# Kernel tuning notes

Hardware: AMD Instinct MI355X
Metric: run time of the kernel (lower is better)

The kernel has to match this reference:

```python
import jax, jax.numpy as jnp
import numpy as np

OUT = 2048        # weight_size[0]
IN_BASE = 2048    # original input features
N_EMBED = 64      # replacements per iteration
IN_TOT = IN_BASE + 2 * N_EMBED  # 2176, weight_size[1]
NNZ_W = 400000
NNZ_B = 1024
BATCH = 8192


def setup_inputs() -> dict:
    key = jax.random.key(0)
    ks = jax.random.split(key, 10)
    return {
        "x": jax.random.normal(ks[0], (BATCH, IN_BASE), dtype=jnp.float32),
        "weight_vals": jax.random.normal(ks[1], (NNZ_W,), dtype=jnp.float32),
        "weight_rows": jax.random.randint(ks[2], (NNZ_W,), 0, OUT, dtype=jnp.int32),
        "weight_cols": jax.random.randint(ks[3], (NNZ_W,), 0, IN_TOT, dtype=jnp.int32),
        "bias_vals": jax.random.normal(ks[4], (NNZ_B,), dtype=jnp.float32),
        "bias_idx": jax.random.randint(ks[5], (NNZ_B,), 0, OUT, dtype=jnp.int32),
        "embed0_vals": jax.random.uniform(ks[6], (N_EMBED,), dtype=jnp.float32),
        "embed0_parents": jax.random.randint(ks[7], (N_EMBED,), 0, IN_BASE, dtype=jnp.int32),
        "embed1_vals": jax.random.uniform(ks[8], (N_EMBED,), dtype=jnp.float32),
        "embed1_parents": jax.random.randint(ks[9], (N_EMBED,), 0, IN_BASE + N_EMBED, dtype=jnp.int32),
    }


def reference(x, weight_vals, weight_rows, weight_cols, bias_vals, bias_idx,
              embed0_vals, embed0_parents, embed1_vals, embed1_parents):
    # EmbedLinear layers: each appends one new feature per stored row,
    # new_feat[:, c] = value[c] * x[:, parent[c]]  (single nnz per sparse row)
    x = jnp.concatenate([x, x[:, embed0_parents] * embed0_vals[None, :]], axis=1)  # [B, 2112]
    x = jnp.concatenate([x, x[:, embed1_parents] * embed1_vals[None, :]], axis=1)  # [B, 2176]
    # sparse weight -> dense via scatter-add (coalesce semantics sum duplicates)
    W = jnp.zeros((OUT, IN_TOT), dtype=weight_vals.dtype).at[weight_rows, weight_cols].add(weight_vals)
    b = jnp.zeros((OUT,), dtype=bias_vals.dtype).at[bias_idx].add(bias_vals)
    # (W @ x^T)^T + b  ==  x @ W^T + b
    return x @ W.T + b[None, :]
```

## Files before the change

kernel.cpp:

```cpp
#include <hip/hip_runtime.h>
#include <stdint.h>

#define OUT_F   2048
#define IN_BASE 2048
#define N_EMB   64
#define IN_TOT  2176
#define NNZ_W   400000
#define NNZ_B   1024
#define BATCH   8192

typedef __bf16 bf16x8 __attribute__((ext_vector_type(8)));
typedef __bf16 bf16x4 __attribute__((ext_vector_type(4)));
typedef float  floatx16 __attribute__((ext_vector_type(16)));

__global__ void __launch_bounds__(256) build_x_kernel(
    const float* __restrict__ x,
    const float* __restrict__ e0v, const int* __restrict__ e0p,
    const float* __restrict__ e1v, const int* __restrict__ e1p,
    __bf16* __restrict__ xb)
{
    const int GROUPS = IN_TOT / 4;
    int gid = blockIdx.x * 256 + threadIdx.x;
    int b = gid / GROUPS;
    int g = gid - b * GROUPS;
    const float* xr = x + (size_t)b * IN_BASE;

    float v[4];
    if (g < IN_BASE / 4) {
        const float4 t = *(const float4*)(xr + g * 4);
        v[0] = t.x; v[1] = t.y; v[2] = t.z; v[3] = t.w;
    } else if (g < (IN_BASE + N_EMB) / 4) {
        int j = (g - IN_BASE / 4) * 4;
#pragma unroll
        for (int t = 0; t < 4; t++) v[t] = e0v[j + t] * xr[e0p[j + t]];
    } else {
        int j = (g - (IN_BASE + N_EMB) / 4) * 4;
#pragma unroll
        for (int t = 0; t < 4; t++) {
            int p = e1p[j + t];
            float base = (p < IN_BASE) ? xr[p]
                                       : e0v[p - IN_BASE] * xr[e0p[p - IN_BASE]];
            v[t] = e1v[j + t] * base;
        }
    }
    bf16x4 o;
    o[0] = (__bf16)v[0]; o[1] = (__bf16)v[1]; o[2] = (__bf16)v[2]; o[3] = (__bf16)v[3];
    *(bf16x4*)(xb + (size_t)b * IN_TOT + g * 4) = o;
}

__global__ void __launch_bounds__(256) scatter_kernel(
    const float* __restrict__ wv, const int* __restrict__ wr,
    const int* __restrict__ wc,
    const float* __restrict__ bv, const int* __restrict__ bi,
    float* __restrict__ Wf, float* __restrict__ bf)
{
    int i = blockIdx.x * 256 + threadIdx.x;
    if (i < NNZ_W) {
        atomicAdd(Wf + (size_t)wr[i] * IN_TOT + wc[i], wv[i]);
    } else if (i < NNZ_W + NNZ_B) {
        int j = i - NNZ_W;
        atomicAdd(bf + bi[j], bv[j]);
    }
}

__global__ void __launch_bounds__(256) w_to_bf16_kernel(
    const float* __restrict__ Wf, __bf16* __restrict__ Wb)
{
    int e = (blockIdx.x * 256 + threadIdx.x) * 4;
    const float4 t = *(const float4*)(Wf + e);
    bf16x4 o;
    o[0] = (__bf16)t.x; o[1] = (__bf16)t.y; o[2] = (__bf16)t.z; o[3] = (__bf16)t.w;
    *(bf16x4*)(Wb + e) = o;
}

#define BM 128
#define BN 128
#define BK 64

__global__ void __launch_bounds__(256) gemm_kernel(
    const __bf16* __restrict__ A,
    const __bf16* __restrict__ W,
    const float*  __restrict__ bias,
    float* __restrict__ C)
{
    __shared__ __bf16 sA[BM * BK];
    __shared__ __bf16 sB[BN * BK];

    const int tid   = threadIdx.x;
    const int bm    = blockIdx.x;
    const int bn    = blockIdx.y;
    const int wave  = tid >> 6;
    const int lane  = tid & 63;
    const int wm    = (wave >> 1) * 64;
    const int wn    = (wave & 1) * 64;
    const int l32   = lane & 31;
    const int khalf = lane >> 5;

    floatx16 acc[2][2] = {};

    const int srow   = tid >> 3;
    const int kchunk = ((tid & 7) ^ ((tid >> 3) & 7)) * 8;
    const __bf16* Ag = A + (size_t)(bm * BM + srow) * IN_TOT + kchunk;
    const __bf16* Wg = W + (size_t)(bn * BN + srow) * IN_TOT + kchunk;
    char* sAb = (char*)sA;
    char* sBb = (char*)sB;

    for (int k0 = 0; k0 < IN_TOT; k0 += BK) {
#pragma unroll
        for (int i = 0; i < 4; i++) {
            __builtin_amdgcn_global_load_lds(
                (__attribute__((address_space(1))) void*)(uintptr_t)(Ag + (size_t)i * 32 * IN_TOT + k0),
                (__attribute__((address_space(3))) void*)(sAb + i * 4096 + tid * 16),
                16, 0, 0);
            __builtin_amdgcn_global_load_lds(
                (__attribute__((address_space(1))) void*)(uintptr_t)(Wg + (size_t)i * 32 * IN_TOT + k0),
                (__attribute__((address_space(3))) void*)(sBb + i * 4096 + tid * 16),
                16, 0, 0);
        }
        __syncthreads();

#pragma unroll
        for (int ks = 0; ks < 4; ks++) {
            const int sl = ((ks * 2 + khalf) ^ (l32 & 7)) * 8;
            bf16x8 af[2], bfr[2];
#pragma unroll
            for (int mi = 0; mi < 2; mi++)
                af[mi] = *(const bf16x8*)(sA + (wm + mi * 32 + l32) * BK + sl);
#pragma unroll
            for (int ni = 0; ni < 2; ni++)
                bfr[ni] = *(const bf16x8*)(sB + (wn + ni * 32 + l32) * BK + sl);
#pragma unroll
            for (int mi = 0; mi < 2; mi++)
#pragma unroll
                for (int ni = 0; ni < 2; ni++)
                    acc[mi][ni] = __builtin_amdgcn_mfma_f32_32x32x16_bf16(
                        af[mi], bfr[ni], acc[mi][ni], 0, 0, 0);
        }
        __syncthreads();
    }

#pragma unroll
    for (int mi = 0; mi < 2; mi++) {
#pragma unroll
        for (int ni = 0; ni < 2; ni++) {
            const int colg = bn * BN + wn + ni * 32 + l32;
            const float bv = bias[colg];
            const int rowb = bm * BM + wm + mi * 32 + 4 * khalf;
#pragma unroll
            for (int reg = 0; reg < 16; reg++) {
                const int rowg = rowb + (reg & 3) + 8 * (reg >> 2);
                C[(size_t)rowg * OUT_F + colg] = acc[mi][ni][reg] + bv;
            }
        }
    }
}

extern "C" void kernel_launch(void* const* d_in, const int* in_sizes, int n_in,
                              void* d_out, int out_size, void* d_ws, size_t ws_size,
                              hipStream_t stream) {
    const float* x      = (const float*)d_in[0];
    const float* w_vals = (const float*)d_in[1];
    const int*   w_rows = (const int*)  d_in[2];
    const int*   w_cols = (const int*)  d_in[3];
    const float* b_vals = (const float*)d_in[4];
    const int*   b_idx  = (const int*)  d_in[5];
    const float* e0v    = (const float*)d_in[6];
    const int*   e0p    = (const int*)  d_in[7];
    const float* e1v    = (const float*)d_in[8];
    const int*   e1p    = (const int*)  d_in[9];
    float* out = (float*)d_out;

    char* ws = (char*)d_ws;
    const size_t W_F32_BYTES  = (size_t)OUT_F * IN_TOT * 4;
    const size_t B_F32_BYTES  = (size_t)OUT_F * 4;
    const size_t W_BF16_BYTES = (size_t)OUT_F * IN_TOT * 2;
    float*  Wf = (float*)ws;
    float*  bf = (float*)(ws + W_F32_BYTES);
    __bf16* Wb = (__bf16*)(ws + W_F32_BYTES + B_F32_BYTES);
    __bf16* xb = (__bf16*)(ws + W_F32_BYTES + B_F32_BYTES + W_BF16_BYTES);

    hipMemsetAsync(Wf, 0, W_F32_BYTES + B_F32_BYTES, stream);

    build_x_kernel<<<(BATCH * (IN_TOT / 4)) / 256, 256, 0, stream>>>(
        x, e0v, e0p, e1v, e1p, xb);

    scatter_kernel<<<(NNZ_W + NNZ_B + 255) / 256, 256, 0, stream>>>(
        w_vals, w_rows, w_cols, b_vals, b_idx, Wf, bf);

    w_to_bf16_kernel<<<((size_t)OUT_F * IN_TOT / 4) / 256, 256, 0, stream>>>(Wf, Wb);

    dim3 grid(BATCH / BM, OUT_F / BN);
    gemm_kernel<<<grid, 256, 0, stream>>>(xb, Wb, bf, out);
}
```

Before: 249.3 us.

## Fuse prep kernels and rebuild GEMM as 256x256 double-buffered 8-wave pipeline

Merges the x-build and scatter kernels into one launch and switches the atomics to unsafeAtomicAdd, which allows hardware float atomics. Rewrites the GEMM with 256x256 tiles, 512 threads and two LDS buffers. Global-to-LDS loads for upcoming K-tiles are interleaved with MFMA phases under fine-grained barriers and s_setprio, to hide load latency and raise arithmetic intensity. The larger tiles use 128KB of LDS per block and give only 256 blocks, so occupancy is low and tail balance gets worse.

Measured after the change: 260.7 us. 4.6% more time.

```diff
diff --git a/kernel.cpp b/kernel.cpp
--- a/kernel.cpp
+++ b/kernel.cpp
@@ -13,53 +13,58 @@
 typedef __bf16 bf16x4 __attribute__((ext_vector_type(4)));
 typedef float  floatx16 __attribute__((ext_vector_type(16)));
 
-__global__ void __launch_bounds__(256) build_x_kernel(
+#define AS1 __attribute__((address_space(1)))
+#define AS3 __attribute__((address_space(3)))
+
+#define NB_BUILD (BATCH * (IN_TOT / 4) / 256)
+#define NB_SCAT  ((NNZ_W + NNZ_B + 255) / 256)
+
+__global__ void __launch_bounds__(256) prep_kernel(
     const float* __restrict__ x,
     const float* __restrict__ e0v, const int* __restrict__ e0p,
     const float* __restrict__ e1v, const int* __restrict__ e1p,
-    __bf16* __restrict__ xb)
-{
-    const int GROUPS = IN_TOT / 4;
-    int gid = blockIdx.x * 256 + threadIdx.x;
-    int b = gid / GROUPS;
-    int g = gid - b * GROUPS;
-    const float* xr = x + (size_t)b * IN_BASE;
-
-    float v[4];
-    if (g < IN_BASE / 4) {
-        const float4 t = *(const float4*)(xr + g * 4);
-        v[0] = t.x; v[1] = t.y; v[2] = t.z; v[3] = t.w;
-    } else if (g < (IN_BASE + N_EMB) / 4) {
-        int j = (g - IN_BASE / 4) * 4;
-#pragma unroll
-        for (int t = 0; t < 4; t++) v[t] = e0v[j + t] * xr[e0p[j + t]];
-    } else {
-        int j = (g - (IN_BASE + N_EMB) / 4) * 4;
-#pragma unroll
-        for (int t = 0; t < 4; t++) {
-            int p = e1p[j + t];
-            float base = (p < IN_BASE) ? xr[p]
-                                       : e0v[p - IN_BASE] * xr[e0p[p - IN_BASE]];
-            v[t] = e1v[j + t] * base;
-        }
-    }
-    bf16x4 o;
-    o[0] = (__bf16)v[0]; o[1] = (__bf16)v[1]; o[2] = (__bf16)v[2]; o[3] = (__bf16)v[3];
-    *(bf16x4*)(xb + (size_t)b * IN_TOT + g * 4) = o;
-}
-
-__global__ void __launch_bounds__(256) scatter_kernel(
+    __bf16* __restrict__ xb,
     const float* __restrict__ wv, const int* __restrict__ wr,
     const int* __restrict__ wc,
     const float* __restrict__ bv, const int* __restrict__ bi,
-    float* __restrict__ Wf, float* __restrict__ bf)
+    float* __restrict__ Wf, float* __restrict__ bfp)
 {
-    int i = blockIdx.x * 256 + threadIdx.x;
-    if (i < NNZ_W) {
-        atomicAdd(Wf + (size_t)wr[i] * IN_TOT + wc[i], wv[i]);
-    } else if (i < NNZ_W + NNZ_B) {
-        int j = i - NNZ_W;
-        atomicAdd(bf + bi[j], bv[j]);
+    if (blockIdx.x < NB_BUILD) {
+        const int GROUPS = IN_TOT / 4;
+        int gid = blockIdx.x * 256 + threadIdx.x;
+        int b = gid / GROUPS;
+        int g = gid - b * GROUPS;
+        const float* xr = x + (size_t)b * IN_BASE;
+
+        float v[4];
+        if (g < IN_BASE / 4) {
+            const float4 t = *(const float4*)(xr + g * 4);
+            v[0] = t.x; v[1] = t.y; v[2] = t.z; v[3] = t.w;
+        } else if (g < (IN_BASE + N_EMB) / 4) {
+            int j = (g - IN_BASE / 4) * 4;
+#pragma unroll
+            for (int t = 0; t < 4; t++) v[t] = e0v[j + t] * xr[e0p[j + t]];
+        } else {
+            int j = (g - (IN_BASE + N_EMB) / 4) * 4;
+#pragma unroll
+            for (int t = 0; t < 4; t++) {
+                int p = e1p[j + t];
+                float base = (p < IN_BASE) ? xr[p]
+                                           : e0v[p - IN_BASE] * xr[e0p[p - IN_BASE]];
+                v[t] = e1v[j + t] * base;
+            }
+        }
+        bf16x4 o;
+        o[0] = (__bf16)v[0]; o[1] = (__bf16)v[1]; o[2] = (__bf16)v[2]; o[3] = (__bf16)v[3];
+        *(bf16x4*)(xb + (size_t)b * IN_TOT + g * 4) = o;
+    } else {
+        int i = (blockIdx.x - NB_BUILD) * 256 + threadIdx.x;
+        if (i < NNZ_W) {
+            unsafeAtomicAdd(Wf + (size_t)wr[i] * IN_TOT + wc[i], wv[i]);
+        } else if (i < NNZ_W + NNZ_B) {
+            int j = i - NNZ_W;
+            unsafeAtomicAdd(bfp + bi[j], bv[j]);
+        }
     }
 }
 
@@ -73,84 +78,122 @@
     *(bf16x4*)(Wb + e) = o;
 }
 
-#define BM 128
-#define BN 128
+#define BM 256
+#define BN 256
 #define BK 64
-
-__global__ void __launch_bounds__(256) gemm_kernel(
+#define NKT (IN_TOT / BK)
+static_assert(NKT % 2 == 0, "pipeline consumes K-tiles in pairs");
+
+#define CFENCE asm volatile("" ::: "memory")
+#define BAR do { CFENCE; __builtin_amdgcn_s_barrier(); CFENCE; } while (0)
+#define VMW(n) asm volatile("s_waitcnt vmcnt(" #n ")" ::: "memory")
+#define NOPS do {} while (0)
+
+#define STAGE(G, SBC, buf, tile, half) do {                                     \
+    const __bf16* _s = (G) + (size_t)((half) * 128) * IN_TOT + (tile) * 64;     \
+    char* _d = (SBC) + (buf) * 32768 + (half) * 16384 + tid * 16;               \
+    __builtin_amdgcn_global_load_lds((AS1 void*)(uintptr_t)_s,                  \
+                                     (AS3 void*)_d, 16, 0, 0);                  \
+    __builtin_amdgcn_global_load_lds((AS1 void*)(uintptr_t)(_s + (size_t)64 * IN_TOT), \
+                                     (AS3 void*)(_d + 8192), 16, 0, 0);         \
+} while (0)
+
+#define PHASE(buf, m, n, STG, WT) do {                                          \
+    const __bf16* _pA = sA + (buf) * 16384;                                     \
+    const __bf16* _pB = sB + (buf) * 16384;                                     \
+    bf16x8 _af[2][4], _bv[4];                                                   \
+    _Pragma("unroll") for (int ks = 0; ks < 4; ks++) {                          \
+        const int kc = ks * 2 + khalf;                                          \
+        _Pragma("unroll") for (int mi = 0; mi < 2; mi++) {                      \
+            const int r = (m) * 128 + wm * 64 + mi * 32 + l32;                  \
+            _af[mi][ks] = *(const bf16x8*)(_pA + r * 64 + ((kc ^ (r & 7)) * 8));\
+        }                                                                       \
+        const int rb = (n) * 128 + wn * 32 + l32;                               \
+        _bv[ks] = *(const bf16x8*)(_pB + rb * 64 + ((kc ^ (rb & 7)) * 8));      \
+    }                                                                           \
+    STG;                                                                        \
+    WT;                                                                         \
+    BAR;                                                                        \
+    __builtin_amdgcn_s_setprio(1);                                              \
+    _Pragma("unroll") for (int mi = 0; mi < 2; mi++)                            \
+        _Pragma("unroll") for (int ks = 0; ks < 4; ks++)                        \
+            acc[m][mi][n] = __builtin_amdgcn_mfma_f32_32x32x16_bf16(            \
+                _af[mi][ks], _bv[ks], acc[m][mi][n], 0, 0, 0);                  \
+    __builtin_amdgcn_s_setprio(0);                                              \
+    BAR;                                                                        \
+} while (0)
+
+__global__ void __launch_bounds__(512, 2) gemm_kernel(
     const __bf16* __restrict__ A,
     const __bf16* __restrict__ W,
     const float*  __restrict__ bias,
     float* __restrict__ C)
 {
-    __shared__ __bf16 sA[BM * BK];
-    __shared__ __bf16 sB[BN * BK];
+    __shared__ __align__(16) __bf16 sA[2 * 256 * 64];
+    __shared__ __align__(16) __bf16 sB[2 * 256 * 64];
 
     const int tid   = threadIdx.x;
     const int bm    = blockIdx.x;
     const int bn    = blockIdx.y;
     const int wave  = tid >> 6;
     const int lane  = tid & 63;
-    const int wm    = (wave >> 1) * 64;
-    const int wn    = (wave & 1) * 64;
+    const int wm    = wave >> 2;
+    const int wn    = wave & 3;
     const int l32   = lane & 31;
     const int khalf = lane >> 5;
 
-    floatx16 acc[2][2] = {};
+    floatx16 acc[2][2][2] = {};
 
     const int srow   = tid >> 3;
     const int kchunk = ((tid & 7) ^ ((tid >> 3) & 7)) * 8;
     const __bf16* Ag = A + (size_t)(bm * BM + srow) * IN_TOT + kchunk;
     const __bf16* Wg = W + (size_t)(bn * BN + srow) * IN_TOT + kchunk;
-    char* sAb = (char*)sA;
-    char* sBb = (char*)sB;
-
-    for (int k0 = 0; k0 < IN_TOT; k0 += BK) {
-#pragma unroll
-        for (int i = 0; i < 4; i++) {
-            __builtin_amdgcn_global_load_lds(
-                (__attribute__((address_space(1))) void*)(uintptr_t)(Ag + (size_t)i * 32 * IN_TOT + k0),
-                (__attribute__((address_space(3))) void*)(sAb + i * 4096 + tid * 16),
-                16, 0, 0);
-            __builtin_amdgcn_global_load_lds(
-                (__attribute__((address_space(1))) void*)(uintptr_t)(Wg + (size_t)i * 32 * IN_TOT + k0),
-                (__attribute__((address_space(3))) void*)(sBb + i * 4096 + tid * 16),
-                16, 0, 0);
-        }
-        __syncthreads();
-
-#pragma unroll
-        for (int ks = 0; ks < 4; ks++) {
-            const int sl = ((ks * 2 + khalf) ^ (l32 & 7)) * 8;
-            bf16x8 af[2], bfr[2];
-#pragma unroll
-            for (int mi = 0; mi < 2; mi++)
-                af[mi] = *(const bf16x8*)(sA + (wm + mi * 32 + l32) * BK + sl);
-#pragma unroll
-            for (int ni = 0; ni < 2; ni++)
-                bfr[ni] = *(const bf16x8*)(sB + (wn + ni * 32 + l32) * BK + sl);
-#pragma unroll
-            for (int mi = 0; mi < 2; mi++)
-#pragma unroll
-                for (int ni = 0; ni < 2; ni++)
-                    acc[mi][ni] = __builtin_amdgcn_mfma_f32_32x32x16_bf16(
-                        af[mi], bfr[ni], acc[mi][ni], 0, 0, 0);
-        }
-        __syncthreads();
+    char* sAc = (char*)sA;
+    char* sBc = (char*)sB;
+
+    STAGE(Ag, sAc, 0, 0, 0);
+    STAGE(Ag, sAc, 0, 0, 1);
+    STAGE(Wg, sBc, 0, 0, 0);
+    STAGE(Wg, sBc, 0, 0, 1);
+    STAGE(Ag, sAc, 1, 1, 0);
+    STAGE(Wg, sBc, 1, 1, 1);
+    VMW(4);
+    BAR;
+
+#pragma unroll 1
+    for (int i = 0; i < NKT / 2 - 1; ++i) {
+        const int t1 = 2 * i + 1, t2 = 2 * i + 2, t3 = 2 * i + 3;
+        PHASE(0, 0, 0, STAGE(Ag, sAc, 1, t1, 1), NOPS);
+        PHASE(0, 0, 1, STAGE(Wg, sBc, 1, t1, 0), NOPS);
+        PHASE(0, 1, 1, STAGE(Ag, sAc, 0, t2, 0), NOPS);
+        PHASE(0, 1, 0, STAGE(Wg, sBc, 0, t2, 1), VMW(4));
+        PHASE(1, 0, 0, STAGE(Ag, sAc, 0, t2, 1), NOPS);
+        PHASE(1, 0, 1, STAGE(Wg, sBc, 0, t2, 0), NOPS);
+        PHASE(1, 1, 1, STAGE(Ag, sAc, 1, t3, 0), NOPS);
+        PHASE(1, 1, 0, STAGE(Wg, sBc, 1, t3, 1), VMW(4));
     }
-
-#pragma unroll
-    for (int mi = 0; mi < 2; mi++) {
-#pragma unroll
-        for (int ni = 0; ni < 2; ni++) {
-            const int colg = bn * BN + wn + ni * 32 + l32;
-            const float bv = bias[colg];
-            const int rowb = bm * BM + wm + mi * 32 + 4 * khalf;
-#pragma unroll
-            for (int reg = 0; reg < 16; reg++) {
-                const int rowg = rowb + (reg & 3) + 8 * (reg >> 2);
-                C[(size_t)rowg * OUT_F + colg] = acc[mi][ni][reg] + bv;
-            }
+    PHASE(0, 0, 0, STAGE(Ag, sAc, 1, NKT - 1, 1), NOPS);
+    PHASE(0, 0, 1, STAGE(Wg, sBc, 1, NKT - 1, 0), NOPS);
+    PHASE(0, 1, 1, NOPS, NOPS);
+    PHASE(0, 1, 0, NOPS, VMW(0));
+    PHASE(1, 0, 0, NOPS, NOPS);
+    PHASE(1, 0, 1, NOPS, NOPS);
+    PHASE(1, 1, 1, NOPS, NOPS);
+    PHASE(1, 1, 0, NOPS, NOPS);
+
+#pragma unroll
+    for (int m = 0; m < 2; m++)
+#pragma unroll
+    for (int mi = 0; mi < 2; mi++)
+#pragma unroll
+    for (int n = 0; n < 2; n++) {
+        const int colg = bn * BN + n * 128 + wn * 32 + l32;
+        const float bvv = bias[colg];
+        const int rowb = bm * BM + m * 128 + wm * 64 + mi * 32 + 4 * khalf;
+#pragma unroll
+        for (int reg = 0; reg < 16; reg++) {
+            const int rowg = rowb + (reg & 3) + 8 * (reg >> 2);
+            C[(size_t)rowg * OUT_F + colg] = acc[m][mi][n][reg] + bvv;
         }
     }
 }
@@ -175,20 +218,18 @@
     const size_t B_F32_BYTES  = (size_t)OUT_F * 4;
     const size_t W_BF16_BYTES = (size_t)OUT_F * IN_TOT * 2;
     float*  Wf = (float*)ws;
-    float*  bf = (float*)(ws + W_F32_BYTES);
+    float*  bfp = (float*)(ws + W_F32_BYTES);
     __bf16* Wb = (__bf16*)(ws + W_F32_BYTES + B_F32_BYTES);
     __bf16* xb = (__bf16*)(ws + W_F32_BYTES + B_F32_BYTES + W_BF16_BYTES);
 
     hipMemsetAsync(Wf, 0, W_F32_BYTES + B_F32_BYTES, stream);
 
-    build_x_kernel<<<(BATCH * (IN_TOT / 4)) / 256, 256, 0, stream>>>(
-        x, e0v, e0p, e1v, e1p, xb);
-
-    scatter_kernel<<<(NNZ_W + NNZ_B + 255) / 256, 256, 0, stream>>>(
-        w_vals, w_rows, w_cols, b_vals, b_idx, Wf, bf);
+    prep_kernel<<<NB_BUILD + NB_SCAT, 256, 0, stream>>>(
+        x, e0v, e0p, e1v, e1p, xb,
+        w_vals, w_rows, w_cols, b_vals, b_idx, Wf, bfp);
 
     w_to_bf16_kernel<<<((size_t)OUT_F * IN_TOT / 4) / 256, 256, 0, stream>>>(Wf, Wb);
 
     dim3 grid(BATCH / BM, OUT_F / BN);
-    gemm_kernel<<<grid, 256, 0, stream>>>(xb, Wb, bf, out);
-}
+    gemm_kernel<<<grid, 512, 0, stream>>>(xb, Wb, bfp, out);
+}
```
